# Kernel optimization log

Measured on AMD Instinct MI355X. Metric: run time of the kernel, lower is better.

## Reference

```python
import jax, jax.numpy as jnp
import numpy as np

D_MODEL = 1024
NUM_HEADS = 16
HEAD_DIM = D_MODEL // NUM_HEADS


def setup_inputs() -> dict:
    key = jax.random.key(0)
    ks = jax.random.split(key, 11)
    S, B, D = 2048, 2, D_MODEL
    scale = 1.0 / np.sqrt(D)
    inp = {
        'query': jax.random.normal(ks[0], (S, B, D), dtype=jnp.float32),
        'key': jax.random.normal(ks[1], (S, B, D), dtype=jnp.float32),
        'value': jax.random.normal(ks[2], (S, B, D), dtype=jnp.float32),
        'Wq': jax.random.normal(ks[3], (D, D), dtype=jnp.float32) * scale,
        'bq': jnp.zeros((D,), dtype=jnp.float32),
        'Wk': jax.random.normal(ks[4], (D, D), dtype=jnp.float32) * scale,
        'bk': jnp.zeros((D,), dtype=jnp.float32),
        'Wv': jax.random.normal(ks[5], (D, D), dtype=jnp.float32) * scale,
        'bv': jnp.zeros((D,), dtype=jnp.float32),
        'Wo': jax.random.normal(ks[6], (D, D), dtype=jnp.float32) * scale,
        'bo': jnp.zeros((D,), dtype=jnp.float32),
    }
    return inp


def reference(query, key, value, Wq, bq, Wk, bk, Wv, bv, Wo, bo):
    # query/key/value: [S, B, D] (seq-first, as in the torch module)
    S, B, D = query.shape
    H, Hd = NUM_HEADS, HEAD_DIM
    # Linear: x @ W.T + b (torch convention), then split heads -> [B, H, S, Hd]
    def proj_heads(x, W, b):
        y = jnp.einsum('sbd,ed->sbe', x, W) + b  # [S, B, D]
        return y.reshape(x.shape[0], B, H, Hd).transpose(1, 2, 0, 3)
    q = proj_heads(query, Wq, bq)   # [B, H, S, Hd]
    k = proj_heads(key, Wk, bk)     # [B, H, Sk, Hd]
    v = proj_heads(value, Wv, bv)   # [B, H, Sk, Hd]
    scores = jnp.einsum('bhsd,bhtd->bhst', q, k) / jnp.sqrt(jnp.asarray(Hd, q.dtype))
    probs = jax.nn.softmax(scores, axis=-1)  # dropout p=0.0 -> identity
    attn = jnp.einsum('bhst,bhtd->bhsd', probs, v)  # [B, H, S, Hd]
    attn = attn.transpose(2, 0, 1, 3).reshape(S, B, D)  # [S, B, D]
    out = jnp.einsum('sbd,ed->sbe', attn, Wo) + bo
    return out
```

## Files before the change

### kernel.cpp

```cpp
#include <hip/hip_runtime.h>
#include <stdint.h>

#define S_LEN 2048
#define BATCH 2
#define DM    1024
#define NH    16
#define HD    64
#define MROWS 4096

typedef float f32x4 __attribute__((ext_vector_type(4)));
typedef short bfrag __attribute__((ext_vector_type(8)));
typedef unsigned short u16x4_t __attribute__((ext_vector_type(4)));
typedef unsigned short u16x8_t __attribute__((ext_vector_type(8)));
typedef int i32x4_t __attribute__((ext_vector_type(4)));

#define EXP2F(x) __builtin_amdgcn_exp2f(x)

__device__ inline f32x4 mfma16(bfrag a, bfrag b, f32x4 c) {
    return __builtin_amdgcn_mfma_f32_16x16x32_bf16(a, b, c, 0, 0, 0);
}

__device__ inline unsigned short bf16_rn(float x) {
    unsigned u = __builtin_bit_cast(unsigned, x);
    return (unsigned short)((u + 0x7fffu + ((u >> 16) & 1u)) >> 16);
}

__device__ inline void split_bf16(float x, unsigned short &h, unsigned short &l) {
    unsigned u = __builtin_bit_cast(unsigned, x);
    h = (unsigned short)(u >> 16);
    float hf = __builtin_bit_cast(float, u & 0xffff0000u);
    float r = x - hf;
    l = (unsigned short)(__builtin_bit_cast(unsigned, r) >> 16);
}

__device__ inline unsigned pack_rhu(float a, float b) {
    unsigned ua = __builtin_bit_cast(unsigned, a) + 0x8000u;
    unsigned ub = __builtin_bit_cast(unsigned, b) + 0x8000u;
    return (ua >> 16) | (ub & 0xffff0000u);
}

typedef __attribute__((address_space(1))) const unsigned int as1_u32;
typedef __attribute__((address_space(3))) unsigned int as3_u32;
__device__ inline void async16(void* lds, const void* g) {
    __builtin_amdgcn_global_load_lds((as1_u32*)g, (as3_u32*)lds, 16, 0, 0);
}

__global__ __launch_bounds__(256)
void cvt_kernel(const float* __restrict__ Wq, const float* __restrict__ Wk,
                const float* __restrict__ Wv, const float* __restrict__ Wo,
                unsigned short* __restrict__ Wqb, unsigned short* __restrict__ Wkb,
                unsigned short* __restrict__ Wvb,
                unsigned short* __restrict__ Woh, unsigned short* __restrict__ Wol)
{
    const int z = blockIdx.z;
    size_t idx = ((size_t)blockIdx.x * 256 + threadIdx.x) * 8;
    if (idx >= (size_t)DM * DM) return;
    const float* src = (z == 0) ? Wq : (z == 1) ? Wk : (z == 2) ? Wv : Wo;
    float4 f0 = *(const float4*)&src[idx];
    float4 f1 = *(const float4*)&src[idx + 4];
    if (z < 3) {
        unsigned short* dst = (z == 0) ? Wqb : (z == 1) ? Wkb : Wvb;
        u16x8_t v = { bf16_rn(f0.x), bf16_rn(f0.y), bf16_rn(f0.z), bf16_rn(f0.w),
                      bf16_rn(f1.x), bf16_rn(f1.y), bf16_rn(f1.z), bf16_rn(f1.w) };
        *(u16x8_t*)&dst[idx] = v;
    } else {
        unsigned short h0,h1,h2,h3,h4,h5,h6,h7, l0,l1,l2,l3,l4,l5,l6,l7;
        split_bf16(f0.x,h0,l0); split_bf16(f0.y,h1,l1);
        split_bf16(f0.z,h2,l2); split_bf16(f0.w,h3,l3);
        split_bf16(f1.x,h4,l4); split_bf16(f1.y,h5,l5);
        split_bf16(f1.z,h6,l6); split_bf16(f1.w,h7,l7);
        u16x8_t vh = {h0,h1,h2,h3,h4,h5,h6,h7};
        u16x8_t vl = {l0,l1,l2,l3,l4,l5,l6,l7};
        *(u16x8_t*)&Woh[idx] = vh;
        *(u16x8_t*)&Wol[idx] = vl;
    }
}

__global__ __launch_bounds__(512)
void qkv_gemm(const float* __restrict__ Qin, const float* __restrict__ Kin,
              const float* __restrict__ Vin,
              const unsigned short* __restrict__ Wqb,
              const unsigned short* __restrict__ Wkb,
              const unsigned short* __restrict__ Wvb,
              const float* __restrict__ bq, const float* __restrict__ bk,
              const float* __restrict__ bv,
              unsigned short* __restrict__ Qb, unsigned short* __restrict__ Kb,
              unsigned short* __restrict__ Vt)
{
    __shared__ float          sAf[128*32];
    __shared__ unsigned short sB [128*32];

    const int tid = threadIdx.x, lane = tid & 63, w8 = tid >> 6;
    const int m16 = lane & 15, q4 = lane >> 4;
    const int wr = w8 >> 2, wc = w8 & 3;
    const int z = blockIdx.z;

    int id = blockIdx.x + 8 * blockIdx.y;
    int j  = id >> 3;
    const int m0 = ((id & 7) * 4 + (j & 3)) * 128;
    const int n0 = (j >> 2) * 128;

    const float* A    = (z == 0) ? Qin : (z == 1) ? Kin : Vin;
    const unsigned short* W = (z == 0) ? Wqb : (z == 1) ? Wkb : Wvb;
    const float* bias = (z == 0) ? bq : (z == 1) ? bk : bv;
    unsigned short* outp = (z == 0) ? Qb : (z == 1) ? Kb : Vt;

    const int ar0 = tid >> 3,          ac0 = (tid & 7) ^ (ar0 & 7);
    const int ar1 = (tid + 512) >> 3,  ac1 = ((tid + 512) & 7) ^ (ar1 & 7);
    const float* gA0 = A + (size_t)(m0 + ar0) * DM + ac0 * 4;
    const float* gA1 = A + (size_t)(m0 + ar1) * DM + ac1 * 4;
    const int br = tid >> 2,  bc = (tid & 3) ^ ((br ^ (br >> 2)) & 3);
    const unsigned short* gB = W + (size_t)(n0 + br) * DM + bc * 8;

    float*          ldsA0 = &sAf[w8 * 256];
    float*          ldsA1 = &sAf[2048 + w8 * 256];
    unsigned short* ldsB  = &sB [w8 * 512];

    int offA[4][2], offB[2];
    #pragma unroll
    for (int rt = 0; rt < 4; rt++) {
        int r = wr * 64 + rt * 16 + m16, s = r & 7;
        offA[rt][0] = r * 32 + ((q4 * 2 + 0) ^ s) * 4;
        offA[rt][1] = r * 32 + ((q4 * 2 + 1) ^ s) * 4;
    }
    #pragma unroll
    for (int ct = 0; ct < 2; ct++) {
        int r = wc * 32 + ct * 16 + m16;
        offB[ct] = r * 32 + ((q4 ^ ((r ^ (r >> 2)) & 3)) << 3);
    }

    f32x4 acc[4][2];
    const f32x4 zero4 = {0.f, 0.f, 0.f, 0.f};
    #pragma unroll
    for (int i = 0; i < 4; i++)
        #pragma unroll
        for (int jj = 0; jj < 2; jj++) acc[i][jj] = zero4;

    for (int k0 = 0; k0 < DM; k0 += 32) {
        async16(ldsA0, gA0);
        async16(ldsA1, gA1);
        async16(ldsB,  gB);
        gA0 += 32; gA1 += 32; gB += 32;
        __syncthreads();

        bfrag a[4], bb[2];
        #pragma unroll
        for (int rt = 0; rt < 4; rt++) {
            f32x4 lo = *(const f32x4*)&sAf[offA[rt][0]];
            f32x4 hi = *(const f32x4*)&sAf[offA[rt][1]];
            i32x4_t pk = { (int)pack_rhu(lo.x, lo.y), (int)pack_rhu(lo.z, lo.w),
                           (int)pack_rhu(hi.x, hi.y), (int)pack_rhu(hi.z, hi.w) };
            a[rt] = __builtin_bit_cast(bfrag, pk);
        }
        #pragma unroll
        for (int ct = 0; ct < 2; ct++)
            bb[ct] = *(const bfrag*)&sB[offB[ct]];

        #pragma unroll
        for (int rt = 0; rt < 4; rt++)
            #pragma unroll
            for (int ct = 0; ct < 2; ct++)
                acc[rt][ct] = mfma16(a[rt], bb[ct], acc[rt][ct]);
        __syncthreads();
    }

    const float SCALE = (z == 0) ? 0.18033688011112042f : 1.0f;
    #pragma unroll
    for (int rt = 0; rt < 4; rt++)
        #pragma unroll
        for (int ct = 0; ct < 2; ct++)
            #pragma unroll
            for (int reg = 0; reg < 4; reg++) {
                int r = m0 + wr * 64 + rt * 16 + q4 * 4 + reg;
                int c = n0 + wc * 32 + ct * 16 + m16;
                float v = (acc[rt][ct][reg] + bias[c]) * SCALE;
                int s = r >> 1, b = r & 1, hh = c >> 6, d = c & 63;
                unsigned short bv16 = bf16_rn(v);
                if (z == 2)
                    outp[((size_t)(b * NH + hh) * HD + d) * S_LEN + s] = bv16;
                else
                    outp[((size_t)(b * NH + hh) * S_LEN + s) * HD + d] = bv16;
            }
}

__global__ __launch_bounds__(256)
void attn_kernel(const unsigned short* __restrict__ Qb,
                 const unsigned short* __restrict__ Kb,
                 const unsigned short* __restrict__ Vt,
                 unsigned short* __restrict__ Ap)
{
    __shared__ unsigned short sK[2][64*64];
    __shared__ unsigned short sV[2][64*64];
    __shared__ unsigned int   sPT[4][32*36];

    const int tid = threadIdx.x, lane = tid & 63, w4 = tid >> 6;
    const int m16 = lane & 15, q4 = lane >> 4;

    int id = blockIdx.x;
    int xcd = id & 7, jj = id >> 3;
    const int bh = xcd * 4 + (jj >> 4);
    const int qc = jj & 15;
    const int b = bh >> 4, h = bh & 15;
    const int qw = qc * 128 + w4 * 32;

    const unsigned short* Qp = Qb + (size_t)bh * (S_LEN * HD);
    const unsigned short* Kp = Kb + (size_t)bh * (S_LEN * HD);
    const unsigned short* Vp = Vt + (size_t)bh * (S_LEN * HD);
    unsigned int* pw = sPT[w4];

    bfrag aq[2][2];
    #pragma unroll
    for (int nt = 0; nt < 2; nt++)
        #pragma unroll
        for (int kc = 0; kc < 2; kc++)
            aq[nt][kc] = *(const bfrag*)&Qp[(size_t)(qw + nt*16 + m16) * HD + kc*32 + q4*8];

    const int r0 = tid >> 3,         g0 = (tid & 7) ^ (r0 & 7);
    const int r1 = (tid + 256) >> 3, g1 = (tid & 7) ^ (r1 & 7);
    const char* gK0 = (const char*)Kp + (size_t)r0 * 128  + g0 * 16;
    const char* gK1 = (const char*)Kp + (size_t)r1 * 128  + g1 * 16;
    const char* gV0 = (const char*)Vp + (size_t)r0 * 4096 + g0 * 16;
    const char* gV1 = (const char*)Vp + (size_t)r1 * 4096 + g1 * 16;
    const int ldsw = w4 * 1024;

    const f32x4 zero4 = {0.f, 0.f, 0.f, 0.f};
    f32x4 O[2][4];
    float lp[2] = {0.f, 0.f};
    #pragma unroll
    for (int nt = 0; nt < 2; nt++)
        #pragma unroll
        for (int dt = 0; dt < 4; dt++) O[nt][dt] = zero4;

    async16((char*)sK[0] + ldsw,        gK0);
    async16((char*)sK[0] + 4096 + ldsw, gK1);
    async16((char*)sV[0] + ldsw,        gV0);
    async16((char*)sV[0] + 4096 + ldsw, gV1);

    const int NT = S_LEN / 64;
    for (int it = 0; it < NT; it++) {
        const int bi = it & 1;
        __syncthreads();
        if (it + 1 < NT) {
            size_t ko = (size_t)(it + 1) * 8192, vo = (size_t)(it + 1) * 128;
            async16((char*)sK[bi^1] + ldsw,        gK0 + ko);
            async16((char*)sK[bi^1] + 4096 + ldsw, gK1 + ko);
            async16((char*)sV[bi^1] + ldsw,        gV0 + vo);
            async16((char*)sV[bi^1] + 4096 + ldsw, gV1 + vo);
        }

        const unsigned short* kb = sK[bi];
        const unsigned short* vb = sV[bi];

        bfrag ak[4][2];
        #pragma unroll
        for (int mt = 0; mt < 4; mt++) {
            int r = mt*16 + m16, s = r & 7;
            ak[mt][0] = *(const bfrag*)&kb[r*64 + ((q4     ^ s) << 3)];
            ak[mt][1] = *(const bfrag*)&kb[r*64 + (((4+q4) ^ s) << 3)];
        }

        #pragma unroll
        for (int nt = 0; nt < 2; nt++) {
            f32x4 Sc[4];
            #pragma unroll
            for (int mt = 0; mt < 4; mt++) {
                Sc[mt] = mfma16(ak[mt][0], aq[nt][0], zero4);
                Sc[mt] = mfma16(ak[mt][1], aq[nt][1], Sc[mt]);
            }
            unsigned rowb = (unsigned)(nt*16 + m16) * 36;
            #pragma unroll
            for (int mt = 0; mt < 4; mt++) {
                float p0 = EXP2F(Sc[mt][0]), p1 = EXP2F(Sc[mt][1]);
                float p2 = EXP2F(Sc[mt][2]), p3 = EXP2F(Sc[mt][3]);
                unsigned c0 = pack_rhu(p0, p1);
                unsigned c1 = pack_rhu(p2, p3);
                float u0 = __builtin_bit_cast(float, c0 << 16);
                float u1 = __builtin_bit_cast(float, c0 & 0xffff0000u);
                float u2 = __builtin_bit_cast(float, c1 << 16);
                float u3 = __builtin_bit_cast(float, c1 & 0xffff0000u);
                lp[nt] += (u0 + u1) + (u2 + u3);
                uint2 c2 = { c0, c1 };
                *(uint2*)&pw[rowb + mt*8 + q4*2] = c2;
            }
        }

        bfrag av[4][2];
        #pragma unroll
        for (int dt = 0; dt < 4; dt++) {
            int r = dt*16 + m16, s = r & 7;
            av[dt][0] = *(const bfrag*)&vb[r*64 + ((q4     ^ s) << 3)];
            av[dt][1] = *(const bfrag*)&vb[r*64 + (((4+q4) ^ s) << 3)];
        }

        #pragma unroll
        for (int nt = 0; nt < 2; nt++) {
            bfrag bp[2];
            #pragma unroll
            for (int kc = 0; kc < 2; kc++)
                bp[kc] = __builtin_bit_cast(bfrag,
                    *(const i32x4_t*)&pw[(unsigned)(nt*16 + m16) * 36 + kc*16 + q4*4]);
            #pragma unroll
            for (int dt = 0; dt < 4; dt++) {
                O[nt][dt] = mfma16(av[dt][0], bp[0], O[nt][dt]);
                O[nt][dt] = mfma16(av[dt][1], bp[1], O[nt][dt]);
            }
        }
    }

    #pragma unroll
    for (int nt = 0; nt < 2; nt++) {
        float l = lp[nt];
        l += __shfl_xor(l, 16);
        l += __shfl_xor(l, 32);
        float inv = 1.0f / l;
        int q = qw + nt*16 + m16;
        size_t rb = ((size_t)q * BATCH + b) * DM + h * 64;
        #pragma unroll
        for (int dt = 0; dt < 4; dt++) {
            u16x4_t o = { bf16_rn(O[nt][dt][0] * inv), bf16_rn(O[nt][dt][1] * inv),
                          bf16_rn(O[nt][dt][2] * inv), bf16_rn(O[nt][dt][3] * inv) };
            *(u16x4_t*)&Ap[rb + dt*16 + q4*4] = o;
        }
    }
}

__global__ __launch_bounds__(512)
void out_gemm(const unsigned short* __restrict__ Ap,
              const unsigned short* __restrict__ Woh,
              const unsigned short* __restrict__ Wol,
              const float* __restrict__ bo, float* __restrict__ out)
{
    __shared__ unsigned short sA[128*32];
    __shared__ unsigned short sH[128*32];
    __shared__ unsigned short sL[128*32];

    const int tid = threadIdx.x, lane = tid & 63, w8 = tid >> 6;
    const int m16 = lane & 15, q4 = lane >> 4;
    const int wr = w8 >> 2, wc = w8 & 3;

    int id = blockIdx.x + 8 * blockIdx.y;
    int j  = id >> 3;
    const int m0 = ((id & 7) * 4 + (j & 3)) * 128;
    const int n0 = (j >> 2) * 128;

    const int br = tid >> 2,  bc = (tid & 3) ^ ((br ^ (br >> 2)) & 3);
    const unsigned short* gA = Ap  + (size_t)(m0 + br) * DM + bc * 8;
    const unsigned short* gH = Woh + (size_t)(n0 + br) * DM + bc * 8;
    const unsigned short* gL = Wol + (size_t)(n0 + br) * DM + bc * 8;
    unsigned short* ldsA = &sA[w8 * 512];
    unsigned short* ldsH = &sH[w8 * 512];
    unsigned short* ldsL = &sL[w8 * 512];

    int offA[4], offB[2];
    #pragma unroll
    for (int rt = 0; rt < 4; rt++) {
        int r = wr * 64 + rt * 16 + m16;
        offA[rt] = r * 32 + ((q4 ^ ((r ^ (r >> 2)) & 3)) << 3);
    }
    #pragma unroll
    for (int ct = 0; ct < 2; ct++) {
        int r = wc * 32 + ct * 16 + m16;
        offB[ct] = r * 32 + ((q4 ^ ((r ^ (r >> 2)) & 3)) << 3);
    }

    f32x4 acc[4][2];
    const f32x4 zero4 = {0.f, 0.f, 0.f, 0.f};
    #pragma unroll
    for (int i = 0; i < 4; i++)
        #pragma unroll
        for (int jj = 0; jj < 2; jj++) acc[i][jj] = zero4;

    for (int k0 = 0; k0 < DM; k0 += 32) {
        async16(ldsA, gA);
        async16(ldsH, gH);
        async16(ldsL, gL);
        gA += 32; gH += 32; gL += 32;
        __syncthreads();

        bfrag a[4], bh2[2], bl2[2];
        #pragma unroll
        for (int rt = 0; rt < 4; rt++) a[rt] = *(const bfrag*)&sA[offA[rt]];
        #pragma unroll
        for (int ct = 0; ct < 2; ct++) {
            bh2[ct] = *(const bfrag*)&sH[offB[ct]];
            bl2[ct] = *(const bfrag*)&sL[offB[ct]];
        }
        #pragma unroll
        for (int rt = 0; rt < 4; rt++)
            #pragma unroll
            for (int ct = 0; ct < 2; ct++) {
                acc[rt][ct] = mfma16(a[rt], bh2[ct], acc[rt][ct]);
                acc[rt][ct] = mfma16(a[rt], bl2[ct], acc[rt][ct]);
            }
        __syncthreads();
    }

    #pragma unroll
    for (int rt = 0; rt < 4; rt++)
        #pragma unroll
        for (int ct = 0; ct < 2; ct++)
            #pragma unroll
            for (int reg = 0; reg < 4; reg++) {
                int r = m0 + wr * 64 + rt * 16 + q4 * 4 + reg;
                int c = n0 + wc * 32 + ct * 16 + m16;
                out[(size_t)r * DM + c] = acc[rt][ct][reg] + bo[c];
            }
}

extern "C" void kernel_launch(void* const* d_in, const int* in_sizes, int n_in,
                              void* d_out, int out_size, void* d_ws, size_t ws_size,
                              hipStream_t stream)
{
    const float* query = (const float*)d_in[0];
    const float* key   = (const float*)d_in[1];
    const float* value = (const float*)d_in[2];
    const float* Wq    = (const float*)d_in[3];
    const float* bq    = (const float*)d_in[4];
    const float* Wk    = (const float*)d_in[5];
    const float* bk    = (const float*)d_in[6];
    const float* Wv    = (const float*)d_in[7];
    const float* bv    = (const float*)d_in[8];
    const float* Wo    = (const float*)d_in[9];
    const float* bo    = (const float*)d_in[10];

    char* ws = (char*)d_ws;
    const size_t MB = 1u << 20;
    unsigned short* Qb  = (unsigned short*)(ws);
    unsigned short* Kb  = (unsigned short*)(ws +  8*MB);
    unsigned short* Vt  = (unsigned short*)(ws + 16*MB);
    unsigned short* Woh = (unsigned short*)(ws + 24*MB);
    unsigned short* Wol = (unsigned short*)(ws + 26*MB);
    unsigned short* Wqb = (unsigned short*)(ws + 28*MB);
    unsigned short* Wkb = (unsigned short*)(ws + 30*MB);
    unsigned short* Wvb = (unsigned short*)(ws + 32*MB);
    unsigned short* Ap  = (unsigned short*)(ws + 28*MB);

    cvt_kernel<<<dim3(512, 1, 4), 256, 0, stream>>>(
        Wq, Wk, Wv, Wo, Wqb, Wkb, Wvb, Woh, Wol);
    qkv_gemm<<<dim3(8, 32, 3), 512, 0, stream>>>(
        query, key, value, Wqb, Wkb, Wvb, bq, bk, bv, Qb, Kb, Vt);
    attn_kernel<<<dim3(512), 256, 0, stream>>>(Qb, Kb, Vt, Ap);
    out_gemm<<<dim3(8, 32), 512, 0, stream>>>(Ap, Woh, Wol, bo, (float*)d_out);
}
```

Baseline: 256.3 us.

## Pre-convert QKV activations to bf16 and use 4-wave QKV GEMM

Result: faster. 243.8 us (-4.9%).

```diff
diff --git a/kernel.cpp b/kernel.cpp
--- a/kernel.cpp
+++ b/kernel.cpp
@@ -48,18 +48,25 @@
 __global__ __launch_bounds__(256)
 void cvt_kernel(const float* __restrict__ Wq, const float* __restrict__ Wk,
                 const float* __restrict__ Wv, const float* __restrict__ Wo,
+                const float* __restrict__ Qin, const float* __restrict__ Kin,
+                const float* __restrict__ Vin,
                 unsigned short* __restrict__ Wqb, unsigned short* __restrict__ Wkb,
                 unsigned short* __restrict__ Wvb,
-                unsigned short* __restrict__ Woh, unsigned short* __restrict__ Wol)
+                unsigned short* __restrict__ Woh, unsigned short* __restrict__ Wol,
+                unsigned short* __restrict__ Qa,  unsigned short* __restrict__ Ka,
+                unsigned short* __restrict__ Va)
 {
     const int z = blockIdx.z;
     size_t idx = ((size_t)blockIdx.x * 256 + threadIdx.x) * 8;
-    if (idx >= (size_t)DM * DM) return;
-    const float* src = (z == 0) ? Wq : (z == 1) ? Wk : (z == 2) ? Wv : Wo;
+    const size_t limit = (z < 4) ? (size_t)DM * DM : (size_t)MROWS * DM;
+    if (idx >= limit) return;
+    const float* src = (z == 0) ? Wq : (z == 1) ? Wk : (z == 2) ? Wv :
+                       (z == 3) ? Wo : (z == 4) ? Qin : (z == 5) ? Kin : Vin;
     float4 f0 = *(const float4*)&src[idx];
     float4 f1 = *(const float4*)&src[idx + 4];
-    if (z < 3) {
-        unsigned short* dst = (z == 0) ? Wqb : (z == 1) ? Wkb : Wvb;
+    if (z != 3) {
+        unsigned short* dst = (z == 0) ? Wqb : (z == 1) ? Wkb : (z == 2) ? Wvb :
+                              (z == 4) ? Qa  : (z == 5) ? Ka  : Va;
         u16x8_t v = { bf16_rn(f0.x), bf16_rn(f0.y), bf16_rn(f0.z), bf16_rn(f0.w),
                       bf16_rn(f1.x), bf16_rn(f1.y), bf16_rn(f1.z), bf16_rn(f1.w) };
         *(u16x8_t*)&dst[idx] = v;
@@ -76,9 +83,10 @@
     }
 }
 
-__global__ __launch_bounds__(512)
-void qkv_gemm(const float* __restrict__ Qin, const float* __restrict__ Kin,
-              const float* __restrict__ Vin,
+__global__ __launch_bounds__(256)
+void qkv_gemm(const unsigned short* __restrict__ Qa,
+              const unsigned short* __restrict__ Ka,
+              const unsigned short* __restrict__ Va,
               const unsigned short* __restrict__ Wqb,
               const unsigned short* __restrict__ Wkb,
               const unsigned short* __restrict__ Wvb,
@@ -87,12 +95,12 @@
               unsigned short* __restrict__ Qb, unsigned short* __restrict__ Kb,
               unsigned short* __restrict__ Vt)
 {
-    __shared__ float          sAf[128*32];
-    __shared__ unsigned short sB [128*32];
-
-    const int tid = threadIdx.x, lane = tid & 63, w8 = tid >> 6;
+    __shared__ unsigned short sA[128*32];
+    __shared__ unsigned short sB[128*32];
+
+    const int tid = threadIdx.x, lane = tid & 63, w4 = tid >> 6;
     const int m16 = lane & 15, q4 = lane >> 4;
-    const int wr = w8 >> 2, wc = w8 & 3;
+    const int wr = w4 >> 1, wc = w4 & 1;
     const int z = blockIdx.z;
 
     int id = blockIdx.x + 8 * blockIdx.y;
@@ -100,66 +108,60 @@
     const int m0 = ((id & 7) * 4 + (j & 3)) * 128;
     const int n0 = (j >> 2) * 128;
 
-    const float* A    = (z == 0) ? Qin : (z == 1) ? Kin : Vin;
+    const unsigned short* A = (z == 0) ? Qa : (z == 1) ? Ka : Va;
     const unsigned short* W = (z == 0) ? Wqb : (z == 1) ? Wkb : Wvb;
     const float* bias = (z == 0) ? bq : (z == 1) ? bk : bv;
     unsigned short* outp = (z == 0) ? Qb : (z == 1) ? Kb : Vt;
 
-    const int ar0 = tid >> 3,          ac0 = (tid & 7) ^ (ar0 & 7);
-    const int ar1 = (tid + 512) >> 3,  ac1 = ((tid + 512) & 7) ^ (ar1 & 7);
-    const float* gA0 = A + (size_t)(m0 + ar0) * DM + ac0 * 4;
-    const float* gA1 = A + (size_t)(m0 + ar1) * DM + ac1 * 4;
-    const int br = tid >> 2,  bc = (tid & 3) ^ ((br ^ (br >> 2)) & 3);
-    const unsigned short* gB = W + (size_t)(n0 + br) * DM + bc * 8;
-
-    float*          ldsA0 = &sAf[w8 * 256];
-    float*          ldsA1 = &sAf[2048 + w8 * 256];
-    unsigned short* ldsB  = &sB [w8 * 512];
-
-    int offA[4][2], offB[2];
+    const int G1 = tid + 256;
+    const int r0 = tid >> 2, g0 = (tid & 3) ^ ((r0 ^ (r0 >> 2)) & 3);
+    const int r1 = G1  >> 2, g1 = (G1  & 3) ^ ((r1 ^ (r1 >> 2)) & 3);
+    const char* gA0 = (const char*)A + (size_t)(m0 + r0) * 2048 + g0 * 16;
+    const char* gA1 = (const char*)A + (size_t)(m0 + r1) * 2048 + g1 * 16;
+    const char* gB0 = (const char*)W + (size_t)(n0 + r0) * 2048 + g0 * 16;
+    const char* gB1 = (const char*)W + (size_t)(n0 + r1) * 2048 + g1 * 16;
+    char* ldsA0 = (char*)sA + w4 * 1024;
+    char* ldsA1 = (char*)sA + 4096 + w4 * 1024;
+    char* ldsB0 = (char*)sB + w4 * 1024;
+    char* ldsB1 = (char*)sB + 4096 + w4 * 1024;
+
+    int offA[4], offB[4];
     #pragma unroll
     for (int rt = 0; rt < 4; rt++) {
-        int r = wr * 64 + rt * 16 + m16, s = r & 7;
-        offA[rt][0] = r * 32 + ((q4 * 2 + 0) ^ s) * 4;
-        offA[rt][1] = r * 32 + ((q4 * 2 + 1) ^ s) * 4;
-    }
-    #pragma unroll
-    for (int ct = 0; ct < 2; ct++) {
-        int r = wc * 32 + ct * 16 + m16;
+        int r = wr * 64 + rt * 16 + m16;
+        offA[rt] = r * 32 + ((q4 ^ ((r ^ (r >> 2)) & 3)) << 3);
+    }
+    #pragma unroll
+    for (int ct = 0; ct < 4; ct++) {
+        int r = wc * 64 + ct * 16 + m16;
         offB[ct] = r * 32 + ((q4 ^ ((r ^ (r >> 2)) & 3)) << 3);
     }
 
-    f32x4 acc[4][2];
+    f32x4 acc[4][4];
     const f32x4 zero4 = {0.f, 0.f, 0.f, 0.f};
     #pragma unroll
     for (int i = 0; i < 4; i++)
         #pragma unroll
-        for (int jj = 0; jj < 2; jj++) acc[i][jj] = zero4;
+        for (int jj = 0; jj < 4; jj++) acc[i][jj] = zero4;
 
     for (int k0 = 0; k0 < DM; k0 += 32) {
         async16(ldsA0, gA0);
         async16(ldsA1, gA1);
-        async16(ldsB,  gB);
-        gA0 += 32; gA1 += 32; gB += 32;
+        async16(ldsB0, gB0);
+        async16(ldsB1, gB1);
+        gA0 += 64; gA1 += 64; gB0 += 64; gB1 += 64;
         __syncthreads();
 
-        bfrag a[4], bb[2];
-        #pragma unroll
-        for (int rt = 0; rt < 4; rt++) {
-            f32x4 lo = *(const f32x4*)&sAf[offA[rt][0]];
-            f32x4 hi = *(const f32x4*)&sAf[offA[rt][1]];
-            i32x4_t pk = { (int)pack_rhu(lo.x, lo.y), (int)pack_rhu(lo.z, lo.w),
-                           (int)pack_rhu(hi.x, hi.y), (int)pack_rhu(hi.z, hi.w) };
-            a[rt] = __builtin_bit_cast(bfrag, pk);
-        }
-        #pragma unroll
-        for (int ct = 0; ct < 2; ct++)
-            bb[ct] = *(const bfrag*)&sB[offB[ct]];
+        bfrag a[4], bb[4];
+        #pragma unroll
+        for (int rt = 0; rt < 4; rt++) a[rt]  = *(const bfrag*)&sA[offA[rt]];
+        #pragma unroll
+        for (int ct = 0; ct < 4; ct++) bb[ct] = *(const bfrag*)&sB[offB[ct]];
 
         #pragma unroll
         for (int rt = 0; rt < 4; rt++)
             #pragma unroll
-            for (int ct = 0; ct < 2; ct++)
+            for (int ct = 0; ct < 4; ct++)
                 acc[rt][ct] = mfma16(a[rt], bb[ct], acc[rt][ct]);
         __syncthreads();
     }
@@ -168,11 +170,11 @@
     #pragma unroll
     for (int rt = 0; rt < 4; rt++)
         #pragma unroll
-        for (int ct = 0; ct < 2; ct++)
+        for (int ct = 0; ct < 4; ct++)
             #pragma unroll
             for (int reg = 0; reg < 4; reg++) {
                 int r = m0 + wr * 64 + rt * 16 + q4 * 4 + reg;
-                int c = n0 + wc * 32 + ct * 16 + m16;
+                int c = n0 + wc * 64 + ct * 16 + m16;
                 float v = (acc[rt][ct][reg] + bias[c]) * SCALE;
                 int s = r >> 1, b = r & 1, hh = c >> 6, d = c & 63;
                 unsigned short bv16 = bf16_rn(v);
@@ -433,12 +435,16 @@
     unsigned short* Wqb = (unsigned short*)(ws + 28*MB);
     unsigned short* Wkb = (unsigned short*)(ws + 30*MB);
     unsigned short* Wvb = (unsigned short*)(ws + 32*MB);
+    unsigned short* Va  = (unsigned short*)(ws + 34*MB);
     unsigned short* Ap  = (unsigned short*)(ws + 28*MB);
-
-    cvt_kernel<<<dim3(512, 1, 4), 256, 0, stream>>>(
-        Wq, Wk, Wv, Wo, Wqb, Wkb, Wvb, Woh, Wol);
-    qkv_gemm<<<dim3(8, 32, 3), 512, 0, stream>>>(
-        query, key, value, Wqb, Wkb, Wvb, bq, bk, bv, Qb, Kb, Vt);
+    unsigned short* Qa  = (unsigned short*)d_out;
+    unsigned short* Ka  = (unsigned short*)d_out + (size_t)MROWS*DM;
+
+    cvt_kernel<<<dim3(2048, 1, 7), 256, 0, stream>>>(
+        Wq, Wk, Wv, Wo, query, key, value,
+        Wqb, Wkb, Wvb, Woh, Wol, Qa, Ka, Va);
+    qkv_gemm<<<dim3(8, 32, 3), 256, 0, stream>>>(
+        Qa, Ka, Va, Wqb, Wkb, Wvb, bq, bk, bv, Qb, Kb, Vt);
     attn_kernel<<<dim3(512), 256, 0, stream>>>(Qb, Kb, Vt, Ap);
     out_gemm<<<dim3(8, 32), 512, 0, stream>>>(Ap, Woh, Wol, bo, (float*)d_out);
 }
```
